# Kernel tuning notes

Measured on AMD Instinct MI355X. Metric: run time of the kernel, lower is better.

Reference implementation:

```python
import jax, jax.numpy as jnp
import numpy as np

N = 50000        # nodes
E = 1600000      # edges (avg degree 32)
INDIM = 256
OUTDIM = 64
HEADS = 4


def setup_inputs() -> dict:
    key = jax.random.key(0)
    k = jax.random.split(key, 7)
    h = jax.random.normal(k[0], (N, INDIM), dtype=jnp.float32)
    e = jax.random.normal(k[1], (E, 1), dtype=jnp.float32)
    norm = jax.random.uniform(k[2], (N, 1), dtype=jnp.float32)
    src = jax.random.randint(k[3], (E,), 0, N)
    dst = jax.random.randint(k[4], (E,), 0, N)
    # per-head params: W: Linear(indim->outdim, bias=False); a: Linear(2*outdim->1, bias=False)
    W = jax.random.normal(k[5], (HEADS, INDIM, OUTDIM), dtype=jnp.float32) * 0.05
    a = jax.random.normal(k[6], (HEADS, 2 * OUTDIM), dtype=jnp.float32) * 0.05
    return {"h": h, "e": e, "norm": norm, "src": src, "dst": dst, "W": W, "a": a}


def reference(h, e, norm, src, dst, W, a):
    n = h.shape[0]
    h_in = h
    hs = h * norm                      # [N, indim]
    head_outs = []
    for i in range(HEADS):             # small fixed head count
        z = hs @ W[i]                  # [N, outdim]
        # attn score: a^T [z_src ; z_dst] decomposed into per-node halves
        s_src = z @ a[i, :OUTDIM]      # [N]
        s_dst = z @ a[i, OUTDIM:]      # [N]
        score = s_src[src] + s_dst[dst]                      # [E]
        # segment softmax over incoming edges of each dst node
        m = jax.ops.segment_max(score, dst, num_segments=n)  # [N]
        m = jnp.where(jnp.isfinite(m), m, 0.0)
        ex = jnp.exp(score - m[dst])                         # [E]
        den = jax.ops.segment_sum(ex, dst, num_segments=n)   # [N]
        alpha = ex / den[dst]                                # [E]
        # scatter-weighted sum of source features
        hh = jax.ops.segment_sum(alpha[:, None] * z[src], dst, num_segments=n)  # [N, outdim]
        head_outs.append(hh * norm)
    hout = jnp.concatenate(head_outs, axis=1)   # [N, outdim*heads] == [N, indim]
    return (h_in + hout, e)
```

## Files before the change

kernel.cpp:

```cpp
#include <hip/hip_runtime.h>

#define NN 50000
#define NE 1600000
#define IND 256
#define OUTD 64
#define NH 4
#define EPB 4096
#define NBLKP 391
#define NBUCK 196

typedef __attribute__((ext_vector_type(8))) short short8;
typedef __attribute__((ext_vector_type(4))) float f32x4;

__device__ __forceinline__ unsigned short f2bf(float x) {
    unsigned int u = __float_as_uint(x);
    u = (u + 0x7FFFu + ((u >> 16) & 1u)) >> 16;
    return (unsigned short)u;
}
__device__ __forceinline__ float bf2f(unsigned short u) {
    return __uint_as_float((unsigned int)u << 16);
}

__global__ __launch_bounds__(256) void k_wt(const float* __restrict__ W, unsigned short* __restrict__ Wtf,
                                            const float4* __restrict__ e4, float4* __restrict__ oute4) {
    int t = blockIdx.x * 256 + threadIdx.x;
    int e = t & 7;
    int lane = (t >> 3) & 63;
    int ks = (t >> 9) & 7;
    int nt = (t >> 12) & 3;
    int hd = (t >> 14) & 3;
    int k = ks * 32 + (lane >> 4) * 8 + e;
    int d = nt * 16 + (lane & 15);
    Wtf[t] = f2bf(W[hd * IND * OUTD + k * OUTD + d]);
    for (int i = t; i < NE / 4; i += 65536) oute4[i] = e4[i];
}

__global__ __launch_bounds__(256) void k_gmm(const float* __restrict__ h, const float* __restrict__ norm,
                                             const unsigned short* __restrict__ Wtf, const float* __restrict__ a,
                                             unsigned short* __restrict__ zb,
                                             float* __restrict__ ssrc, float* __restrict__ sdst) {
    __shared__ unsigned short ldsA[32 * 264];
    __shared__ unsigned short ldsE[4][16 * 80];
    const int tid = threadIdx.x;
    const int lane = tid & 63;
    const int wv = tid >> 6;
    const int m0 = blockIdx.x * 32;
    const int c0 = wv * 64;
    const int r16 = lane & 15, kg = lane >> 4;

    #pragma unroll
    for (int q = 0; q < 4; ++q) {
        int idx = q * 2048 + tid * 8;
        int row = idx >> 8, col = idx & 255;
        int grow = m0 + row; if (grow > NN - 1) grow = NN - 1;
        float nmv = norm[grow];
        const float4* hp = (const float4*)(h + (size_t)grow * IND + col);
        float4 x0 = hp[0], x1 = hp[1];
        short8 r;
        r[0] = (short)f2bf(x0.x * nmv); r[1] = (short)f2bf(x0.y * nmv);
        r[2] = (short)f2bf(x0.z * nmv); r[3] = (short)f2bf(x0.w * nmv);
        r[4] = (short)f2bf(x1.x * nmv); r[5] = (short)f2bf(x1.y * nmv);
        r[6] = (short)f2bf(x1.z * nmv); r[7] = (short)f2bf(x1.w * nmv);
        *(short8*)&ldsA[row * 264 + col] = r;
    }
    __syncthreads();

    const short8* bfp = (const short8*)(Wtf) + (size_t)wv * 4 * 8 * 64;

    f32x4 acc[2][4] = {};
    #pragma unroll
    for (int ks = 0; ks < 8; ++ks) {
        short8 av0 = *(const short8*)&ldsA[r16 * 264 + ks * 32 + kg * 8];
        short8 av1 = *(const short8*)&ldsA[(16 + r16) * 264 + ks * 32 + kg * 8];
        #pragma unroll
        for (int nt = 0; nt < 4; ++nt) {
            short8 cb = bfp[(nt * 8 + ks) * 64 + lane];
            acc[0][nt] = __builtin_amdgcn_mfma_f32_16x16x32_bf16(av0, cb, acc[0][nt], 0, 0, 0);
            acc[1][nt] = __builtin_amdgcn_mfma_f32_16x16x32_bf16(av1, cb, acc[1][nt], 0, 0, 0);
        }
    }

    float asrc[4], adst[4];
    #pragma unroll
    for (int j = 0; j < 4; ++j) {
        asrc[j] = a[wv * 128 + j * 16 + r16];
        adst[j] = a[wv * 128 + 64 + j * 16 + r16];
    }
    #pragma unroll
    for (int mt = 0; mt < 2; ++mt) {
        #pragma unroll
        for (int r = 0; r < 4; ++r) {
            int row = m0 + mt * 16 + kg * 4 + r;
            unsigned short q0 = f2bf(acc[mt][0][r]);
            unsigned short q1 = f2bf(acc[mt][1][r]);
            unsigned short q2 = f2bf(acc[mt][2][r]);
            unsigned short q3 = f2bf(acc[mt][3][r]);
            float ps = bf2f(q0) * asrc[0] + bf2f(q1) * asrc[1] + bf2f(q2) * asrc[2] + bf2f(q3) * asrc[3];
            float pd = bf2f(q0) * adst[0] + bf2f(q1) * adst[1] + bf2f(q2) * adst[2] + bf2f(q3) * adst[3];
            #pragma unroll
            for (int off = 1; off < 16; off <<= 1) {
                ps += __shfl_xor(ps, off);
                pd += __shfl_xor(pd, off);
            }
            unsigned short* lp = &ldsE[wv][(kg * 4 + r) * 80];
            lp[ 0 + r16] = q0;
            lp[16 + r16] = q1;
            lp[32 + r16] = q2;
            lp[48 + r16] = q3;
            if (row < NN && r16 == 0) {
                ssrc[(row << 2) + wv] = ps;
                sdst[(row << 2) + wv] = pd;
            }
        }
        asm volatile("s_waitcnt lgkmcnt(0)" ::: "memory");
        __builtin_amdgcn_sched_barrier(0);
        #pragma unroll
        for (int hf = 0; hf < 2; ++hf) {
            int lrow = hf * 8 + (lane >> 3);
            int chunk = lane & 7;
            short8 v = *(const short8*)&ldsE[wv][lrow * 80 + chunk * 8];
            int grow = m0 + mt * 16 + lrow;
            if (grow < NN)
                *(short8*)(zb + (size_t)grow * IND + c0 + chunk * 8) = v;
        }
        __builtin_amdgcn_sched_barrier(0);
    }
}

__global__ __launch_bounds__(256) void k_phist(const int* __restrict__ dst, int* __restrict__ bh) {
    __shared__ int lh[NBUCK];
    int tid = threadIdx.x;
    if (tid < NBUCK) lh[tid] = 0;
    __syncthreads();
    int base = blockIdx.x * EPB;
    for (int i = tid; i < EPB; i += 256) {
        int ed = base + i;
        if (ed < NE) atomicAdd(&lh[dst[ed] >> 8], 1);
    }
    __syncthreads();
    if (tid < NBUCK) bh[blockIdx.x * NBUCK + tid] = lh[tid];
}

__global__ __launch_bounds__(256) void k_poffA(const int* __restrict__ bh, int* __restrict__ goff,
                                               int* __restrict__ colsum) {
    __shared__ int wsum[4];
    int t = blockIdx.x;
    int tid = threadIdx.x;
    int b0 = tid * 2, b1 = tid * 2 + 1;
    int v0 = (b0 < NBLKP) ? bh[b0 * NBUCK + t] : 0;
    int v1 = (b1 < NBLKP) ? bh[b1 * NBUCK + t] : 0;
    int s = v0 + v1;
    int lane = tid & 63, w = tid >> 6;
    int x = s;
    #pragma unroll
    for (int off = 1; off < 64; off <<= 1) {
        int tmp = __shfl_up(x, off);
        if (lane >= off) x += tmp;
    }
    if (lane == 63) wsum[w] = x;
    __syncthreads();
    int waveoff = 0;
    for (int j = 0; j < w; ++j) waveoff += wsum[j];
    int excl = waveoff + x - s;
    if (b0 < NBLKP) goff[b0 * NBUCK + t] = excl;
    if (b1 < NBLKP) goff[b1 * NBUCK + t] = excl + v0;
    if (tid == 255) colsum[t] = waveoff + x;
}

__global__ __launch_bounds__(256) void k_poffB(const int* __restrict__ colsum, int* __restrict__ bstart) {
    __shared__ int wsum[4];
    int tid = threadIdx.x;
    int v = (tid < NBUCK) ? colsum[tid] : 0;
    int lane = tid & 63, w = tid >> 6;
    int x = v;
    #pragma unroll
    for (int off = 1; off < 64; off <<= 1) {
        int tmp = __shfl_up(x, off);
        if (lane >= off) x += tmp;
    }
    if (lane == 63) wsum[w] = x;
    __syncthreads();
    int waveoff = 0;
    for (int j = 0; j < w; ++j) waveoff += wsum[j];
    if (tid < NBUCK) bstart[tid] = waveoff + x - v;
    if (tid == 0) bstart[NBUCK] = NE;
}

__global__ __launch_bounds__(256) void k_pscat(const int* __restrict__ src, const int* __restrict__ dst,
                                               const int* __restrict__ goff, const int* __restrict__ bstart,
                                               unsigned int* __restrict__ tmp) {
    __shared__ int lcur[NBUCK];
    __shared__ int bs[NBUCK];
    int tid = threadIdx.x;
    if (tid < NBUCK) { lcur[tid] = 0; bs[tid] = bstart[tid]; }
    __syncthreads();
    int base = blockIdx.x * EPB;
    const int* go = goff + blockIdx.x * NBUCK;
    for (int i = tid; i < EPB; i += 256) {
        int ed = base + i;
        if (ed < NE) {
            int d = dst[ed];
            int bin = d >> 8;
            int r = atomicAdd(&lcur[bin], 1);
            tmp[bs[bin] + go[bin] + r] = ((unsigned int)(d & 255) << 16) | (unsigned int)src[ed];
        }
    }
}

__global__ __launch_bounds__(256) void k_lsort(const unsigned int* __restrict__ tmp,
                                               const int* __restrict__ bstart,
                                               int* __restrict__ rowp, int* __restrict__ srcs) {
    __shared__ int lh[2048], lcur[2048];
    __shared__ int wsum[4];
    int b = blockIdx.x, tid = threadIdx.x;
    int base = bstart[b], cnt = bstart[b + 1] - base;
    #pragma unroll
    for (int j = 0; j < 8; ++j) lh[j * 256 + tid] = 0;
    __syncthreads();
    for (int i = tid; i < cnt; i += 256) {
        unsigned int rec = tmp[base + i];
        int key = ((int)(rec >> 16) << 3) | ((int)(rec & 0xFFFFu) >> 13);
        atomicAdd(&lh[key & 2047], 1);
    }
    __syncthreads();
    int local[8];
    int s = 0;
    #pragma unroll
    for (int j = 0; j < 8; ++j) { local[j] = s; s += lh[tid * 8 + j]; }
    int lane = tid & 63, w = tid >> 6;
    int x = s;
    #pragma unroll
    for (int off = 1; off < 64; off <<= 1) {
        int t2 = __shfl_up(x, off);
        if (lane >= off) x += t2;
    }
    if (lane == 63) wsum[w] = x;
    __syncthreads();
    int waveoff = 0;
    for (int j = 0; j < w; ++j) waveoff += wsum[j];
    int excl = waveoff + x - s;
    #pragma unroll
    for (int j = 0; j < 8; ++j) lcur[tid * 8 + j] = excl + local[j];
    int d = (b << 8) + tid;
    if (d < NN) rowp[d] = base + excl;
    if (b == NBUCK - 1 && tid == 0) rowp[NN] = NE;
    __syncthreads();
    for (int i = tid; i < cnt; i += 256) {
        unsigned int rec = tmp[base + i];
        int srcv = (int)(rec & 0xFFFFu);
        int key = ((int)(rec >> 16) << 3) | (srcv >> 13);
        int p = atomicAdd(&lcur[key & 2047], 1);
        srcs[base + p] = srcv;
    }
}

__global__ __launch_bounds__(256) void k_agg(const unsigned short* __restrict__ zb, const int* __restrict__ rowp,
                                             const int* __restrict__ srcs, const float* __restrict__ ssrc,
                                             const float* __restrict__ sdst,
                                             const float* __restrict__ h, const float* __restrict__ norm,
                                             float* __restrict__ out) {
    int wv = threadIdx.x >> 6, lane = threadIdx.x & 63;
    int half = lane >> 5;
    int l = lane & 31;
    int n = blockIdx.x * 8 + wv * 2 + half;
    if (n >= NN) return;
    int p0 = rowp[n], p1 = rowp[n + 1];
    int deg = p1 - p0;
    int hd = l >> 3;
    float sd = sdst[(n << 2) + hd];
    float a0 = 0.f, a1 = 0.f, a2 = 0.f, a3 = 0.f;
    float a4 = 0.f, a5 = 0.f, a6 = 0.f, a7 = 0.f;
    float b0 = 0.f, b1 = 0.f, b2 = 0.f, b3 = 0.f;
    float b4 = 0.f, b5 = 0.f, b6 = 0.f, b7 = 0.f;
    float denA = 0.f, denB = 0.f;
    int zoffl = l << 3;
    int i = 0;
    int s0, s1, s2, s3;
    float e0, e1, e2, e3;
    uint4 z0, z1, z2, z3;
    if (deg >= 4) {
        s0 = srcs[p0];     s1 = srcs[p0 + 1];
        s2 = srcs[p0 + 2]; s3 = srcs[p0 + 3];
        e0 = ssrc[(s0 << 2) + hd]; e1 = ssrc[(s1 << 2) + hd];
        e2 = ssrc[(s2 << 2) + hd]; e3 = ssrc[(s3 << 2) + hd];
        z0 = *(const uint4*)(zb + (s0 << 8) + zoffl);
        z1 = *(const uint4*)(zb + (s1 << 8) + zoffl);
        z2 = *(const uint4*)(zb + (s2 << 8) + zoffl);
        z3 = *(const uint4*)(zb + (s3 << 8) + zoffl);
    }
    for (; i + 8 <= deg; i += 4) {
        float f0 = e0, f1 = e1, f2 = e2, f3 = e3;
        uint4 y0 = z0, y1 = z1, y2 = z2, y3 = z3;
        int q = p0 + i + 4;
        s0 = srcs[q];     s1 = srcs[q + 1];
        s2 = srcs[q + 2]; s3 = srcs[q + 3];
        e0 = ssrc[(s0 << 2) + hd]; e1 = ssrc[(s1 << 2) + hd];
        e2 = ssrc[(s2 << 2) + hd]; e3 = ssrc[(s3 << 2) + hd];
        z0 = *(const uint4*)(zb + (s0 << 8) + zoffl);
        z1 = *(const uint4*)(zb + (s1 << 8) + zoffl);
        z2 = *(const uint4*)(zb + (s2 << 8) + zoffl);
        z3 = *(const uint4*)(zb + (s3 << 8) + zoffl);
        float w0 = __expf(f0 + sd);
        float w1 = __expf(f1 + sd);
        float w2 = __expf(f2 + sd);
        float w3 = __expf(f3 + sd);
        a0 += w0 * bf2f((unsigned short)(y0.x & 0xFFFFu));
        a1 += w0 * bf2f((unsigned short)(y0.x >> 16));
        a2 += w0 * bf2f((unsigned short)(y0.y & 0xFFFFu));
        a3 += w0 * bf2f((unsigned short)(y0.y >> 16));
        a4 += w0 * bf2f((unsigned short)(y0.z & 0xFFFFu));
        a5 += w0 * bf2f((unsigned short)(y0.z >> 16));
        a6 += w0 * bf2f((unsigned short)(y0.w & 0xFFFFu));
        a7 += w0 * bf2f((unsigned short)(y0.w >> 16));
        denA += w0;
        b0 += w1 * bf2f((unsigned short)(y1.x & 0xFFFFu));
        b1 += w1 * bf2f((unsigned short)(y1.x >> 16));
        b2 += w1 * bf2f((unsigned short)(y1.y & 0xFFFFu));
        b3 += w1 * bf2f((unsigned short)(y1.y >> 16));
        b4 += w1 * bf2f((unsigned short)(y1.z & 0xFFFFu));
        b5 += w1 * bf2f((unsigned short)(y1.z >> 16));
        b6 += w1 * bf2f((unsigned short)(y1.w & 0xFFFFu));
        b7 += w1 * bf2f((unsigned short)(y1.w >> 16));
        denB += w1;
        a0 += w2 * bf2f((unsigned short)(y2.x & 0xFFFFu));
        a1 += w2 * bf2f((unsigned short)(y2.x >> 16));
        a2 += w2 * bf2f((unsigned short)(y2.y & 0xFFFFu));
        a3 += w2 * bf2f((unsigned short)(y2.y >> 16));
        a4 += w2 * bf2f((unsigned short)(y2.z & 0xFFFFu));
        a5 += w2 * bf2f((unsigned short)(y2.z >> 16));
        a6 += w2 * bf2f((unsigned short)(y2.w & 0xFFFFu));
        a7 += w2 * bf2f((unsigned short)(y2.w >> 16));
        denA += w2;
        b0 += w3 * bf2f((unsigned short)(y3.x & 0xFFFFu));
        b1 += w3 * bf2f((unsigned short)(y3.x >> 16));
        b2 += w3 * bf2f((unsigned short)(y3.y & 0xFFFFu));
        b3 += w3 * bf2f((unsigned short)(y3.y >> 16));
        b4 += w3 * bf2f((unsigned short)(y3.z & 0xFFFFu));
        b5 += w3 * bf2f((unsigned short)(y3.z >> 16));
        b6 += w3 * bf2f((unsigned short)(y3.w & 0xFFFFu));
        b7 += w3 * bf2f((unsigned short)(y3.w >> 16));
        denB += w3;
    }
    if (deg >= 4) {
        float w0 = __expf(e0 + sd);
        float w1 = __expf(e1 + sd);
        float w2 = __expf(e2 + sd);
        float w3 = __expf(e3 + sd);
        a0 += w0 * bf2f((unsigned short)(z0.x & 0xFFFFu));
        a1 += w0 * bf2f((unsigned short)(z0.x >> 16));
        a2 += w0 * bf2f((unsigned short)(z0.y & 0xFFFFu));
        a3 += w0 * bf2f((unsigned short)(z0.y >> 16));
        a4 += w0 * bf2f((unsigned short)(z0.z & 0xFFFFu));
        a5 += w0 * bf2f((unsigned short)(z0.z >> 16));
        a6 += w0 * bf2f((unsigned short)(z0.w & 0xFFFFu));
        a7 += w0 * bf2f((unsigned short)(z0.w >> 16));
        denA += w0;
        b0 += w1 * bf2f((unsigned short)(z1.x & 0xFFFFu));
        b1 += w1 * bf2f((unsigned short)(z1.x >> 16));
        b2 += w1 * bf2f((unsigned short)(z1.y & 0xFFFFu));
        b3 += w1 * bf2f((unsigned short)(z1.y >> 16));
        b4 += w1 * bf2f((unsigned short)(z1.z & 0xFFFFu));
        b5 += w1 * bf2f((unsigned short)(z1.z >> 16));
        b6 += w1 * bf2f((unsigned short)(z1.w & 0xFFFFu));
        b7 += w1 * bf2f((unsigned short)(z1.w >> 16));
        denB += w1;
        a0 += w2 * bf2f((unsigned short)(z2.x & 0xFFFFu));
        a1 += w2 * bf2f((unsigned short)(z2.x >> 16));
        a2 += w2 * bf2f((unsigned short)(z2.y & 0xFFFFu));
        a3 += w2 * bf2f((unsigned short)(z2.y >> 16));
        a4 += w2 * bf2f((unsigned short)(z2.z & 0xFFFFu));
        a5 += w2 * bf2f((unsigned short)(z2.z >> 16));
        a6 += w2 * bf2f((unsigned short)(z2.w & 0xFFFFu));
        a7 += w2 * bf2f((unsigned short)(z2.w >> 16));
        denA += w2;
        b0 += w3 * bf2f((unsigned short)(z3.x & 0xFFFFu));
        b1 += w3 * bf2f((unsigned short)(z3.x >> 16));
        b2 += w3 * bf2f((unsigned short)(z3.y & 0xFFFFu));
        b3 += w3 * bf2f((unsigned short)(z3.y >> 16));
        b4 += w3 * bf2f((unsigned short)(z3.z & 0xFFFFu));
        b5 += w3 * bf2f((unsigned short)(z3.z >> 16));
        b6 += w3 * bf2f((unsigned short)(z3.w & 0xFFFFu));
        b7 += w3 * bf2f((unsigned short)(z3.w >> 16));
        denB += w3;
        i += 4;
    }
    for (; i < deg; ++i) {
        int st = srcs[p0 + i];
        float w0 = __expf(ssrc[(st << 2) + hd] + sd);
        uint4 zt = *(const uint4*)(zb + (st << 8) + zoffl);
        a0 += w0 * bf2f((unsigned short)(zt.x & 0xFFFFu));
        a1 += w0 * bf2f((unsigned short)(zt.x >> 16));
        a2 += w0 * bf2f((unsigned short)(zt.y & 0xFFFFu));
        a3 += w0 * bf2f((unsigned short)(zt.y >> 16));
        a4 += w0 * bf2f((unsigned short)(zt.z & 0xFFFFu));
        a5 += w0 * bf2f((unsigned short)(zt.z >> 16));
        a6 += w0 * bf2f((unsigned short)(zt.w & 0xFFFFu));
        a7 += w0 * bf2f((unsigned short)(zt.w >> 16));
        denA += w0;
    }
    a0 += b0; a1 += b1; a2 += b2; a3 += b3;
    a4 += b4; a5 += b5; a6 += b6; a7 += b7;
    float den = denA + denB;
    float nm = norm[n];
    float inv = (deg > 0) ? nm / den : 0.f;
    size_t bofs = (size_t)n * IND + zoffl;
    float4 h0 = *(const float4*)(h + bofs);
    float4 h1 = *(const float4*)(h + bofs + 4);
    float4 o0, o1;
    o0.x = h0.x + inv * a0; o0.y = h0.y + inv * a1;
    o0.z = h0.z + inv * a2; o0.w = h0.w + inv * a3;
    o1.x = h1.x + inv * a4; o1.y = h1.y + inv * a5;
    o1.z = h1.z + inv * a6; o1.w = h1.w + inv * a7;
    *(float4*)(out + bofs) = o0;
    *(float4*)(out + bofs + 4) = o1;
}

extern "C" void kernel_launch(void* const* d_in, const int* in_sizes, int n_in,
                              void* d_out, int out_size, void* d_ws, size_t ws_size,
                              hipStream_t stream) {
    const float* h    = (const float*)d_in[0];
    const float* e    = (const float*)d_in[1];
    const float* norm = (const float*)d_in[2];
    const int*   src  = (const int*)d_in[3];
    const int*   dst  = (const int*)d_in[4];
    const float* W    = (const float*)d_in[5];
    const float* a    = (const float*)d_in[6];
    float* out = (float*)d_out;

    char* p = (char*)d_ws;
    unsigned short* Wtf = (unsigned short*)p; p += 262144;
    unsigned short* zb = (unsigned short*)p; p += 25600000;
    float* ssrc = (float*)p; p += 800000;
    float* sdst = (float*)p; p += 800000;
    int*   rowp = (int*)p;   p += 200192;
    int*   srcs = (int*)p;   p += 6400000;
    int*   bh   = (int*)p;   p += 307200;
    int*   goff = (int*)p;   p += 307200;
    int*   bstart = (int*)p; p += 4096;
    int*   colsum = (int*)p; p += 4096;
    unsigned int* tmp = (unsigned int*)p; p += 6400000;

    k_wt<<<256, 256, 0, stream>>>(W, Wtf, (const float4*)e, (float4*)(out + (size_t)NN * IND));
    k_gmm<<<1563, 256, 0, stream>>>(h, norm, Wtf, a, zb, ssrc, sdst);
    k_phist<<<NBLKP, 256, 0, stream>>>(dst, bh);
    k_poffA<<<NBUCK, 256, 0, stream>>>(bh, goff, colsum);
    k_poffB<<<1, 256, 0, stream>>>(colsum, bstart);
    k_pscat<<<NBLKP, 256, 0, stream>>>(src, dst, goff, bstart, tmp);
    k_lsort<<<NBUCK, 256, 0, stream>>>(tmp, bstart, rowp, srcs);
    k_agg<<<6250, 256, 0, stream>>>(zb, rowp, srcs, ssrc, sdst, h, norm, out);
}
```

Measured before the change: 200.0 us.

## Pre-convert scaled h to bf16 in MFMA fragment layout via separate kernel

Adds a k_conv kernel that scales h by norm, converts it to bf16 and writes it in an MFMA-fragment-tiled layout. k_gmm then loads A fragments straight from global memory, dropping its LDS staging and __syncthreads. This adds an extra kernel launch plus a 25.6MB write and read round trip through global memory, in exchange for simpler loads in the GEMM. The layout relies on the 16-row tile count dividing NN exactly.

```diff
diff --git a/kernel.cpp b/kernel.cpp
--- a/kernel.cpp
+++ b/kernel.cpp
@@ -8,6 +8,7 @@
 #define EPB 4096
 #define NBLKP 391
 #define NBUCK 196
+#define NTILE 3125
 
 typedef __attribute__((ext_vector_type(8))) short short8;
 typedef __attribute__((ext_vector_type(4))) float f32x4;
@@ -35,11 +36,28 @@
     for (int i = t; i < NE / 4; i += 65536) oute4[i] = e4[i];
 }
 
-__global__ __launch_bounds__(256) void k_gmm(const float* __restrict__ h, const float* __restrict__ norm,
+__global__ __launch_bounds__(256) void k_conv(const float* __restrict__ h, const float* __restrict__ norm,
+                                              unsigned short* __restrict__ hbf) {
+    int t = blockIdx.x * 256 + threadIdx.x;
+    int row = t >> 5;
+    int col = (t & 31) << 3;
+    float nmv = norm[row];
+    const float4* hp = (const float4*)(h + (size_t)row * IND + col);
+    float4 x0 = hp[0], x1 = hp[1];
+    short8 r;
+    r[0] = (short)f2bf(x0.x * nmv); r[1] = (short)f2bf(x0.y * nmv);
+    r[2] = (short)f2bf(x0.z * nmv); r[3] = (short)f2bf(x0.w * nmv);
+    r[4] = (short)f2bf(x1.x * nmv); r[5] = (short)f2bf(x1.y * nmv);
+    r[6] = (short)f2bf(x1.z * nmv); r[7] = (short)f2bf(x1.w * nmv);
+    int tile = row >> 4, r16 = row & 15;
+    int ks = col >> 5, kg = (col >> 3) & 3;
+    *((short8*)hbf + (size_t)(tile * 8 + ks) * 64 + kg * 16 + r16) = r;
+}
+
+__global__ __launch_bounds__(256) void k_gmm(const unsigned short* __restrict__ hbf,
                                              const unsigned short* __restrict__ Wtf, const float* __restrict__ a,
                                              unsigned short* __restrict__ zb,
                                              float* __restrict__ ssrc, float* __restrict__ sdst) {
-    __shared__ unsigned short ldsA[32 * 264];
     __shared__ unsigned short ldsE[4][16 * 80];
     const int tid = threadIdx.x;
     const int lane = tid & 63;
@@ -48,30 +66,17 @@
     const int c0 = wv * 64;
     const int r16 = lane & 15, kg = lane >> 4;
 
-    #pragma unroll
-    for (int q = 0; q < 4; ++q) {
-        int idx = q * 2048 + tid * 8;
-        int row = idx >> 8, col = idx & 255;
-        int grow = m0 + row; if (grow > NN - 1) grow = NN - 1;
-        float nmv = norm[grow];
-        const float4* hp = (const float4*)(h + (size_t)grow * IND + col);
-        float4 x0 = hp[0], x1 = hp[1];
-        short8 r;
-        r[0] = (short)f2bf(x0.x * nmv); r[1] = (short)f2bf(x0.y * nmv);
-        r[2] = (short)f2bf(x0.z * nmv); r[3] = (short)f2bf(x0.w * nmv);
-        r[4] = (short)f2bf(x1.x * nmv); r[5] = (short)f2bf(x1.y * nmv);
-        r[6] = (short)f2bf(x1.z * nmv); r[7] = (short)f2bf(x1.w * nmv);
-        *(short8*)&ldsA[row * 264 + col] = r;
-    }
-    __syncthreads();
-
+    int tile0 = blockIdx.x * 2;
+    int tile1 = tile0 + 1; if (tile1 > NTILE - 1) tile1 = NTILE - 1;
+    const short8* ap0 = (const short8*)hbf + (size_t)tile0 * 8 * 64 + lane;
+    const short8* ap1 = (const short8*)hbf + (size_t)tile1 * 8 * 64 + lane;
     const short8* bfp = (const short8*)(Wtf) + (size_t)wv * 4 * 8 * 64;
 
     f32x4 acc[2][4] = {};
     #pragma unroll
     for (int ks = 0; ks < 8; ++ks) {
-        short8 av0 = *(const short8*)&ldsA[r16 * 264 + ks * 32 + kg * 8];
-        short8 av1 = *(const short8*)&ldsA[(16 + r16) * 264 + ks * 32 + kg * 8];
+        short8 av0 = ap0[ks * 64];
+        short8 av1 = ap1[ks * 64];
         #pragma unroll
         for (int nt = 0; nt < 4; ++nt) {
             short8 cb = bfp[(nt * 8 + ks) * 64 + lane];
@@ -430,6 +435,7 @@
     char* p = (char*)d_ws;
     unsigned short* Wtf = (unsigned short*)p; p += 262144;
     unsigned short* zb = (unsigned short*)p; p += 25600000;
+    unsigned short* hbf = (unsigned short*)p; p += 25600000;
     float* ssrc = (float*)p; p += 800000;
     float* sdst = (float*)p; p += 800000;
     int*   rowp = (int*)p;   p += 200192;
@@ -441,7 +447,8 @@
     unsigned int* tmp = (unsigned int*)p; p += 6400000;
 
     k_wt<<<256, 256, 0, stream>>>(W, Wtf, (const float4*)e, (float4*)(out + (size_t)NN * IND));
-    k_gmm<<<1563, 256, 0, stream>>>(h, norm, Wtf, a, zb, ssrc, sdst);
+    k_conv<<<6250, 256, 0, stream>>>(h, norm, hbf);
+    k_gmm<<<1563, 256, 0, stream>>>(hbf, Wtf, a, zb, ssrc, sdst);
     k_phist<<<NBLKP, 256, 0, stream>>>(dst, bh);
     k_poffA<<<NBUCK, 256, 0, stream>>>(bh, goff, colsum);
     k_poffB<<<1, 256, 0, stream>>>(colsum, bstart);
```

After: 208.5 us. 1.04x slower.
